# Optimization experiments

Measured on AMD Instinct MI355X. Metric: run time of the kernel, lower is better.

The kernel has to match this reference:

```python
import jax, jax.numpy as jnp
import numpy as np

D_MODEL = 768
NUM_HEADS = 12
HEAD_DIM = D_MODEL // NUM_HEADS


def _trunc_normal(key, shape, std):
    # truncated normal in [-3std, 3std], matching torch.nn.init.trunc_normal_
    return jax.random.truncated_normal(key, -3.0, 3.0, shape, dtype=jnp.float32) * std


def setup_inputs() -> dict:
    key = jax.random.key(0)
    kx, kq, kk, kv, ko = jax.random.split(key, 5)
    std = np.sqrt(2.0 / (D_MODEL + D_MODEL))
    x = jax.random.normal(kx, (4, 2048, D_MODEL), dtype=jnp.float32)
    Wq = _trunc_normal(kq, (D_MODEL, D_MODEL), std)
    Wk = _trunc_normal(kk, (D_MODEL, D_MODEL), std)
    Wv = _trunc_normal(kv, (D_MODEL, D_MODEL), std)
    Wo = _trunc_normal(ko, (D_MODEL, D_MODEL), std)
    return {"x": x, "Wq": Wq, "Wk": Wk, "Wv": Wv, "Wo": Wo}


def reference(x, Wq, Wk, Wv, Wo):
    b, s, _ = x.shape
    h, d = NUM_HEADS, HEAD_DIM
    # Linear: einsum 'b s i, o i -> b s o'
    Q = jnp.einsum('bsi,oi->bso', x, Wq).reshape(b, s, h, d).transpose(0, 2, 1, 3)
    K = jnp.einsum('bsi,oi->bso', x, Wk).reshape(b, s, h, d).transpose(0, 2, 1, 3)
    V = jnp.einsum('bsi,oi->bso', x, Wv).reshape(b, s, h, d).transpose(0, 2, 1, 3)
    scores = jnp.einsum('bhqd,bhkd->bhqk', Q, K) / jnp.sqrt(jnp.float32(d))
    causal = jnp.tril(jnp.ones((s, s), dtype=bool))  # (s, s)
    scores = jnp.where(causal, scores, jnp.float32(-jnp.inf))
    attn = jax.nn.softmax(scores, axis=-1)
    out = jnp.einsum('bhqk,bhkd->bhqd', attn, V)  # (b, h, s, d)
    out = out.transpose(0, 2, 1, 3).reshape(b, s, h * d)
    return jnp.einsum('bsi,oi->bso', out, Wo)
```

## Files before the change

### kernel.cpp

```cpp
#include <hip/hip_runtime.h>
#include <hip/hip_bf16.h>

#define SEQ   2048
#define BATCH 4
#define DM    768
#define NH    12
#define HD    64
#define MTOT  (BATCH*SEQ)

typedef short bf16x8 __attribute__((ext_vector_type(8)));
typedef float f32x4  __attribute__((ext_vector_type(4)));

static __device__ __forceinline__ short f2bf(float f) {
  union { __hip_bfloat16 h; short s; } u;
  u.h = __float2bfloat16(f);
  return u.s;
}

static __device__ __forceinline__ void async_cp16(const short* g, short* l) {
  __builtin_amdgcn_global_load_lds(
      (const __attribute__((address_space(1))) void*)g,
      (__attribute__((address_space(3))) void*)l, 16, 0, 0);
}

__global__ void cvt_kernel(const float* __restrict__ in, short* __restrict__ out, int n4) {
  int i = blockIdx.x * blockDim.x + threadIdx.x;
  if (i >= n4) return;
  float4 v = reinterpret_cast<const float4*>(in)[i];
  short4 o;
  o.x = f2bf(v.x); o.y = f2bf(v.y); o.z = f2bf(v.z); o.w = f2bf(v.w);
  reinterpret_cast<short4*>(out)[i] = o;
}

static __device__ __forceinline__ void gemm_lds_core(
    const short* __restrict__ A, const short* __restrict__ W,
    short* As, short* Bs, int m0, int n0, f32x4 acc[4][4])
{
  const int t = threadIdx.x;
  const int lane = t & 63, w = t >> 6;
  const int quad = lane >> 4, lq = lane & 15;
  const int mw = (w & 1) * 64, nw = (w >> 1) * 64;
  const int r0 = t >> 2, c0 = (t & 3) * 8;
  const short* ga0 = A + (size_t)(m0 + r0) * DM + c0;
  const short* ga1 = A + (size_t)(m0 + 64 + r0) * DM + c0;
  const short* gb0 = W + (size_t)(n0 + r0) * DM + c0;
  const short* gb1 = W + (size_t)(n0 + 64 + r0) * DM + c0;
  short* la0 = As + t * 8;
  short* la1 = As + 2048 + t * 8;
  short* lb0 = Bs + t * 8;
  short* lb1 = Bs + 2048 + t * 8;

  for (int k0 = 0; k0 < DM; k0 += 32) {
    async_cp16(ga0 + k0, la0);
    async_cp16(ga1 + k0, la1);
    async_cp16(gb0 + k0, lb0);
    async_cp16(gb1 + k0, lb1);
    __syncthreads();
    bf16x8 af[4], bf[4];
#pragma unroll
    for (int i = 0; i < 4; ++i) {
      af[i] = *(const bf16x8*)(As + (mw + i * 16 + lq) * 32 + quad * 8);
      bf[i] = *(const bf16x8*)(Bs + (nw + i * 16 + lq) * 32 + quad * 8);
    }
#pragma unroll
    for (int mt = 0; mt < 4; ++mt)
#pragma unroll
      for (int nt = 0; nt < 4; ++nt)
        acc[mt][nt] = __builtin_amdgcn_mfma_f32_16x16x32_bf16(af[mt], bf[nt], acc[mt][nt], 0, 0, 0);
    __syncthreads();
  }
}

__global__ __launch_bounds__(256) void qkv_gemm(
    const short* __restrict__ xb, const short* __restrict__ Wall,
    short* __restrict__ Qb, short* __restrict__ Kb, short* __restrict__ VTb)
{
  __shared__ __align__(16) short As[4096], Bs[4096];
  const int m0 = blockIdx.y * 128, n0 = blockIdx.x * 128;
  f32x4 acc[4][4] = {};
  gemm_lds_core(xb, Wall, As, Bs, m0, n0, acc);

  const int t = threadIdx.x;
  const int lane = t & 63, w = t >> 6;
  const int quad = lane >> 4, lq = lane & 15;
  const int mwb = m0 + (w & 1) * 64, nwb = n0 + (w >> 1) * 64;
#pragma unroll
  for (int mt = 0; mt < 4; ++mt)
#pragma unroll
    for (int nt = 0; nt < 4; ++nt) {
      const int n = nwb + nt * 16 + lq;
      const int z = n / DM, nn = n % DM;
      const int h = nn >> 6, d = nn & 63;
      const int mbase = mwb + mt * 16 + quad * 4;
      const int b = mbase >> 11, s0 = mbase & 2047;
      if (z == 2) {
        short4 v;
        v.x = f2bf(acc[mt][nt][0]); v.y = f2bf(acc[mt][nt][1]);
        v.z = f2bf(acc[mt][nt][2]); v.w = f2bf(acc[mt][nt][3]);
        *(short4*)(VTb + ((size_t)(b * NH + h) * HD + d) * SEQ + s0) = v;
      } else {
        short* dst = (z == 0) ? Qb : Kb;
#pragma unroll
        for (int r = 0; r < 4; ++r)
          dst[((size_t)(b * NH + h) * SEQ + s0 + r) * HD + d] = f2bf(acc[mt][nt][r]);
      }
    }
}

__global__ __launch_bounds__(256) void attn_kernel(
    const short* __restrict__ Qb, const short* __restrict__ Kb,
    const short* __restrict__ VTb, short* __restrict__ AOb)
{
  const int bp = blockIdx.x;
  const int bh = bp % 48;
  const int p  = bp / 48;
  const int w  = threadIdx.x >> 6;
  const int lane = threadIdx.x & 63;
  const int quad = lane >> 4, lq = lane & 15;
  int tile;
  if (w == 0) tile = 2 * p;
  else if (w == 1) tile = 63 - 2 * p;
  else if (w == 2) tile = 2 * p + 1;
  else tile = 62 - 2 * p;
  const int wq = tile * 32;
  const int b = bh / NH, h = bh % NH;

  const short* Qh = Qb  + (size_t)bh * SEQ * HD;
  const short* Kh = Kb  + (size_t)bh * SEQ * HD;
  const short* Vh = VTb + (size_t)bh * HD * SEQ;

  bf16x8 qf[2][2];
#pragma unroll
  for (int qt = 0; qt < 2; ++qt)
#pragma unroll
    for (int hh = 0; hh < 2; ++hh)
      qf[qt][hh] = *(const bf16x8*)(Qh + (size_t)(wq + qt * 16 + lq) * HD + hh * 32 + quad * 8);

  f32x4 o[4][2] = {};
  float m_[2] = {-3e38f, -3e38f};
  float l_[2] = {0.0f, 0.0f};
  const float C = 0.18033688011112042f;

  const int kend = wq + 32;
  for (int kb = 0; kb < kend; kb += 64) {
    f32x4 st[2][2][2] = {};
#pragma unroll
    for (int wd = 0; wd < 2; ++wd)
#pragma unroll
      for (int t = 0; t < 2; ++t) {
        const int krow = kb + 32 * wd + 8 * (lq >> 2) + 4 * t + (lq & 3);
        const short* kp = Kh + (size_t)krow * HD + quad * 8;
        bf16x8 k0 = *(const bf16x8*)(kp);
        bf16x8 k1 = *(const bf16x8*)(kp + 32);
        st[wd][t][0] = __builtin_amdgcn_mfma_f32_16x16x32_bf16(k0, qf[0][0], st[wd][t][0], 0, 0, 0);
        st[wd][t][0] = __builtin_amdgcn_mfma_f32_16x16x32_bf16(k1, qf[0][1], st[wd][t][0], 0, 0, 0);
        st[wd][t][1] = __builtin_amdgcn_mfma_f32_16x16x32_bf16(k0, qf[1][0], st[wd][t][1], 0, 0, 0);
        st[wd][t][1] = __builtin_amdgcn_mfma_f32_16x16x32_bf16(k1, qf[1][1], st[wd][t][1], 0, 0, 0);
      }

    float mx[2] = {-3e38f, -3e38f};
#pragma unroll
    for (int wd = 0; wd < 2; ++wd)
#pragma unroll
      for (int t = 0; t < 2; ++t)
#pragma unroll
        for (int qt = 0; qt < 2; ++qt)
#pragma unroll
          for (int r = 0; r < 4; ++r) {
            const int key = kb + 32 * wd + 8 * quad + 4 * t + r;
            const int q   = wq + qt * 16 + lq;
            const float v = (key <= q) ? st[wd][t][qt][r] : -3e38f;
            st[wd][t][qt][r] = v;
            mx[qt] = fmaxf(mx[qt], v);
          }
#pragma unroll
    for (int qt = 0; qt < 2; ++qt) {
      mx[qt] = fmaxf(mx[qt], __shfl_xor(mx[qt], 16));
      mx[qt] = fmaxf(mx[qt], __shfl_xor(mx[qt], 32));
    }

    float alpha[2], rs[2] = {0.0f, 0.0f};
#pragma unroll
    for (int qt = 0; qt < 2; ++qt) {
      const float mn = fmaxf(m_[qt], mx[qt]);
      alpha[qt] = __builtin_amdgcn_exp2f((m_[qt] - mn) * C);
      m_[qt] = mn;
    }
#pragma unroll
    for (int wd = 0; wd < 2; ++wd)
#pragma unroll
      for (int t = 0; t < 2; ++t)
#pragma unroll
        for (int qt = 0; qt < 2; ++qt)
#pragma unroll
          for (int r = 0; r < 4; ++r) {
            const float pv = __builtin_amdgcn_exp2f((st[wd][t][qt][r] - m_[qt]) * C);
            st[wd][t][qt][r] = pv;
            rs[qt] += pv;
          }
#pragma unroll
    for (int qt = 0; qt < 2; ++qt) {
      rs[qt] += __shfl_xor(rs[qt], 16);
      rs[qt] += __shfl_xor(rs[qt], 32);
      l_[qt] = l_[qt] * alpha[qt] + rs[qt];
    }
#pragma unroll
    for (int mt = 0; mt < 4; ++mt)
#pragma unroll
      for (int qt = 0; qt < 2; ++qt)
#pragma unroll
        for (int r = 0; r < 4; ++r)
          o[mt][qt][r] *= alpha[qt];

    bf16x8 pf[2][2];
#pragma unroll
    for (int wd = 0; wd < 2; ++wd)
#pragma unroll
      for (int qt = 0; qt < 2; ++qt) {
        bf16x8 f;
#pragma unroll
        for (int r = 0; r < 4; ++r) {
          f[r]     = f2bf(st[wd][0][qt][r]);
          f[r + 4] = f2bf(st[wd][1][qt][r]);
        }
        pf[wd][qt] = f;
      }

#pragma unroll
    for (int wd = 0; wd < 2; ++wd)
#pragma unroll
      for (int mt = 0; mt < 4; ++mt) {
        bf16x8 vf = *(const bf16x8*)(Vh + (size_t)(mt * 16 + lq) * SEQ + kb + 32 * wd + quad * 8);
        o[mt][0] = __builtin_amdgcn_mfma_f32_16x16x32_bf16(vf, pf[wd][0], o[mt][0], 0, 0, 0);
        o[mt][1] = __builtin_amdgcn_mfma_f32_16x16x32_bf16(vf, pf[wd][1], o[mt][1], 0, 0, 0);
      }
  }

#pragma unroll
  for (int qt = 0; qt < 2; ++qt) {
    const float inv = 1.0f / l_[qt];
    const int q = wq + qt * 16 + lq;
#pragma unroll
    for (int mt = 0; mt < 4; ++mt) {
      short4 v;
      v.x = f2bf(o[mt][qt][0] * inv);
      v.y = f2bf(o[mt][qt][1] * inv);
      v.z = f2bf(o[mt][qt][2] * inv);
      v.w = f2bf(o[mt][qt][3] * inv);
      *(short4*)(AOb + ((size_t)(b * SEQ + q)) * DM + h * HD + mt * 16 + quad * 4) = v;
    }
  }
}

__global__ __launch_bounds__(256) void out_gemm(
    const short* __restrict__ AOb, const short* __restrict__ Wob, float* __restrict__ C)
{
  __shared__ __align__(16) short As[4096], Bs[4096];
  const int m0 = blockIdx.y * 128, n0 = blockIdx.x * 128;
  f32x4 acc[4][4] = {};
  gemm_lds_core(AOb, Wob, As, Bs, m0, n0, acc);

  const int t = threadIdx.x;
  const int lane = t & 63, w = t >> 6;
  const int quad = lane >> 4, lq = lane & 15;
  const int mwb = m0 + (w & 1) * 64, nwb = n0 + (w >> 1) * 64;
#pragma unroll
  for (int mt = 0; mt < 4; ++mt)
#pragma unroll
    for (int nt = 0; nt < 4; ++nt) {
      const int n = nwb + nt * 16 + lq;
      const int mbase = mwb + mt * 16 + quad * 4;
#pragma unroll
      for (int r = 0; r < 4; ++r)
        C[(size_t)(mbase + r) * DM + n] = acc[mt][nt][r];
    }
}

extern "C" void kernel_launch(void* const* d_in, const int* in_sizes, int n_in,
                              void* d_out, int out_size, void* d_ws, size_t ws_size,
                              hipStream_t stream) {
  const float* x  = (const float*)d_in[0];
  const float* Wq = (const float*)d_in[1];
  const float* Wk = (const float*)d_in[2];
  const float* Wv = (const float*)d_in[3];
  const float* Wo = (const float*)d_in[4];
  float* out = (float*)d_out;

  short* xb  = (short*)d_ws;
  short* Wqb = xb  + (size_t)MTOT * DM;
  short* Wkb = Wqb + DM * DM;
  short* Wvb = Wkb + DM * DM;
  short* Wob = Wvb + DM * DM;
  short* Qb  = Wob + DM * DM;
  short* Kb  = Qb  + (size_t)MTOT * DM;
  short* VTb = Kb  + (size_t)MTOT * DM;
  short* AOb = xb;

  cvt_kernel<<<(MTOT * DM / 4 + 255) / 256, 256, 0, stream>>>(x, xb, MTOT * DM / 4);
  cvt_kernel<<<(DM * DM / 4 + 255) / 256, 256, 0, stream>>>(Wq, Wqb, DM * DM / 4);
  cvt_kernel<<<(DM * DM / 4 + 255) / 256, 256, 0, stream>>>(Wk, Wkb, DM * DM / 4);
  cvt_kernel<<<(DM * DM / 4 + 255) / 256, 256, 0, stream>>>(Wv, Wvb, DM * DM / 4);
  cvt_kernel<<<(DM * DM / 4 + 255) / 256, 256, 0, stream>>>(Wo, Wob, DM * DM / 4);

  qkv_gemm<<<dim3(3 * DM / 128, MTOT / 128), 256, 0, stream>>>(xb, Wqb, Qb, Kb, VTb);
  attn_kernel<<<dim3(768), 256, 0, stream>>>(Qb, Kb, VTb, AOb);
  out_gemm<<<dim3(DM / 128, MTOT / 128), 256, 0, stream>>>(AOb, Wob, out);
}
```

Before: 258.7 us.

## Share K/V tiles via LDS across warps in attention and fuse conversion kernels

The attention kernel now stages each 32-key K and V tile into shared memory with async global-to-LDS copies. All four warps in a block read the tile from there instead of each loading it from global memory. Each warp handles two 16-row query tiles, one near the start and one near the end of the sequence, to balance causal work. The five fp32-to-bf16 conversion launches are merged into one kernel to cut launch overhead. The cost is a __syncthreads pair per 32-key step and smaller per-warp query tiles, which lowers MFMA reuse per K load.

```diff
diff --git a/kernel.cpp b/kernel.cpp
--- a/kernel.cpp
+++ b/kernel.cpp
@@ -23,13 +23,22 @@
       (__attribute__((address_space(3))) void*)l, 16, 0, 0);
 }
 
-__global__ void cvt_kernel(const float* __restrict__ in, short* __restrict__ out, int n4) {
+__global__ void cvt5_kernel(const float* __restrict__ x, const float* __restrict__ wq,
+                            const float* __restrict__ wk, const float* __restrict__ wv,
+                            const float* __restrict__ wo, short* __restrict__ dst) {
+  const int NX4 = MTOT * DM / 4, NW4 = DM * DM / 4, TOT4 = NX4 + 4 * NW4;
   int i = blockIdx.x * blockDim.x + threadIdx.x;
-  if (i >= n4) return;
-  float4 v = reinterpret_cast<const float4*>(in)[i];
+  if (i >= TOT4) return;
+  const float* src; int off;
+  if (i < NX4) { src = x; off = i; }
+  else {
+    int j = i - NX4; int sel = j / NW4; off = j - sel * NW4;
+    src = (sel == 0) ? wq : (sel == 1) ? wk : (sel == 2) ? wv : wo;
+  }
+  float4 v = reinterpret_cast<const float4*>(src)[off];
   short4 o;
   o.x = f2bf(v.x); o.y = f2bf(v.y); o.z = f2bf(v.z); o.w = f2bf(v.w);
-  reinterpret_cast<short4*>(out)[i] = o;
+  reinterpret_cast<short4*>(dst)[i] = o;
 }
 
 static __device__ __forceinline__ void gemm_lds_core(
@@ -111,142 +120,172 @@
     const short* __restrict__ Qb, const short* __restrict__ Kb,
     const short* __restrict__ VTb, short* __restrict__ AOb)
 {
+  __shared__ __align__(16) short Ks[32 * 64];
+  __shared__ __align__(16) short Vs[64 * 32];
   const int bp = blockIdx.x;
   const int bh = bp % 48;
-  const int p  = bp / 48;
-  const int w  = threadIdx.x >> 6;
-  const int lane = threadIdx.x & 63;
+  const int g  = bp / 48;
+  const int tid = threadIdx.x;
+  const int w = tid >> 6, lane = tid & 63;
   const int quad = lane >> 4, lq = lane & 15;
-  int tile;
-  if (w == 0) tile = 2 * p;
-  else if (w == 1) tile = 63 - 2 * p;
-  else if (w == 2) tile = 2 * p + 1;
-  else tile = 62 - 2 * p;
-  const int wq = tile * 32;
+  const int tp = 4 * g + w;
   const int b = bh / NH, h = bh % NH;
+  const int q0b = 16 * tp;
+  const int q1b = 2032 - 16 * tp;
+  const int E0 = q0b + 16;
+  const int E1 = q1b + 16;
+  const int Eblk = 2048 - 64 * g;
 
   const short* Qh = Qb  + (size_t)bh * SEQ * HD;
   const short* Kh = Kb  + (size_t)bh * SEQ * HD;
   const short* Vh = VTb + (size_t)bh * HD * SEQ;
 
-  bf16x8 qf[2][2];
-#pragma unroll
-  for (int qt = 0; qt < 2; ++qt)
-#pragma unroll
-    for (int hh = 0; hh < 2; ++hh)
-      qf[qt][hh] = *(const bf16x8*)(Qh + (size_t)(wq + qt * 16 + lq) * HD + hh * 32 + quad * 8);
-
-  f32x4 o[4][2] = {};
-  float m_[2] = {-3e38f, -3e38f};
-  float l_[2] = {0.0f, 0.0f};
-  const float C = 0.18033688011112042f;
-
-  const int kend = wq + 32;
-  for (int kb = 0; kb < kend; kb += 64) {
-    f32x4 st[2][2][2] = {};
-#pragma unroll
-    for (int wd = 0; wd < 2; ++wd)
-#pragma unroll
-      for (int t = 0; t < 2; ++t) {
-        const int krow = kb + 32 * wd + 8 * (lq >> 2) + 4 * t + (lq & 3);
-        const short* kp = Kh + (size_t)krow * HD + quad * 8;
-        bf16x8 k0 = *(const bf16x8*)(kp);
-        bf16x8 k1 = *(const bf16x8*)(kp + 32);
-        st[wd][t][0] = __builtin_amdgcn_mfma_f32_16x16x32_bf16(k0, qf[0][0], st[wd][t][0], 0, 0, 0);
-        st[wd][t][0] = __builtin_amdgcn_mfma_f32_16x16x32_bf16(k1, qf[0][1], st[wd][t][0], 0, 0, 0);
-        st[wd][t][1] = __builtin_amdgcn_mfma_f32_16x16x32_bf16(k0, qf[1][0], st[wd][t][1], 0, 0, 0);
-        st[wd][t][1] = __builtin_amdgcn_mfma_f32_16x16x32_bf16(k1, qf[1][1], st[wd][t][1], 0, 0, 0);
-      }
-
-    float mx[2] = {-3e38f, -3e38f};
-#pragma unroll
-    for (int wd = 0; wd < 2; ++wd)
-#pragma unroll
-      for (int t = 0; t < 2; ++t)
-#pragma unroll
-        for (int qt = 0; qt < 2; ++qt)
+  bf16x8 qf0[2], qf1[2];
+#pragma unroll
+  for (int hh = 0; hh < 2; ++hh) {
+    qf0[hh] = *(const bf16x8*)(Qh + (size_t)(q0b + lq) * HD + hh * 32 + quad * 8);
+    qf1[hh] = *(const bf16x8*)(Qh + (size_t)(q1b + lq) * HD + hh * 32 + quad * 8);
+  }
+
+  f32x4 o0[4] = {}, o1[4] = {};
+  float m0v = -3e38f, m1v = -3e38f;
+  float l0v = 0.0f, l1v = 0.0f;
+  const float Cc = 0.18033688011112042f;
+
+  const short* gK = Kh + (size_t)(tid >> 3) * HD + (tid & 7) * 8;
+  const short* gV = Vh + (size_t)(tid >> 2) * SEQ + (tid & 3) * 8;
+  short* lK = Ks + tid * 8;
+  short* lV = Vs + tid * 8;
+
+  for (int kb = 0; kb < Eblk; kb += 32) {
+    async_cp16(gK + (size_t)kb * HD, lK);
+    async_cp16(gV + kb, lV);
+    __syncthreads();
+    if (kb < E1) {
+      const bool act0 = kb < E0;
+      f32x4 st0[2] = {}, st1[2] = {};
+#pragma unroll
+      for (int t2 = 0; t2 < 2; ++t2) {
+        const int row = 8 * (lq >> 2) + 4 * t2 + (lq & 3);
+        bf16x8 k0 = *(const bf16x8*)(Ks + row * 64 + quad * 8);
+        bf16x8 k1 = *(const bf16x8*)(Ks + row * 64 + 32 + quad * 8);
+        st1[t2] = __builtin_amdgcn_mfma_f32_16x16x32_bf16(k0, qf1[0], st1[t2], 0, 0, 0);
+        st1[t2] = __builtin_amdgcn_mfma_f32_16x16x32_bf16(k1, qf1[1], st1[t2], 0, 0, 0);
+        if (act0) {
+          st0[t2] = __builtin_amdgcn_mfma_f32_16x16x32_bf16(k0, qf0[0], st0[t2], 0, 0, 0);
+          st0[t2] = __builtin_amdgcn_mfma_f32_16x16x32_bf16(k1, qf0[1], st0[t2], 0, 0, 0);
+        }
+      }
+      bf16x8 vf[4];
+#pragma unroll
+      for (int mt = 0; mt < 4; ++mt)
+        vf[mt] = *(const bf16x8*)(Vs + (mt * 16 + lq) * 32 + quad * 8);
+
+      bf16x8 pf1;
+      {
+        const int qv = q1b + lq;
+        float mx = -3e38f;
+#pragma unroll
+        for (int t2 = 0; t2 < 2; ++t2)
 #pragma unroll
           for (int r = 0; r < 4; ++r) {
-            const int key = kb + 32 * wd + 8 * quad + 4 * t + r;
-            const int q   = wq + qt * 16 + lq;
-            const float v = (key <= q) ? st[wd][t][qt][r] : -3e38f;
-            st[wd][t][qt][r] = v;
-            mx[qt] = fmaxf(mx[qt], v);
+            const int key = kb + 8 * quad + 4 * t2 + r;
+            const float v = (key <= qv) ? st1[t2][r] : -3e38f;
+            st1[t2][r] = v;
+            mx = fmaxf(mx, v);
           }
-#pragma unroll
-    for (int qt = 0; qt < 2; ++qt) {
-      mx[qt] = fmaxf(mx[qt], __shfl_xor(mx[qt], 16));
-      mx[qt] = fmaxf(mx[qt], __shfl_xor(mx[qt], 32));
-    }
-
-    float alpha[2], rs[2] = {0.0f, 0.0f};
-#pragma unroll
-    for (int qt = 0; qt < 2; ++qt) {
-      const float mn = fmaxf(m_[qt], mx[qt]);
-      alpha[qt] = __builtin_amdgcn_exp2f((m_[qt] - mn) * C);
-      m_[qt] = mn;
-    }
-#pragma unroll
-    for (int wd = 0; wd < 2; ++wd)
-#pragma unroll
-      for (int t = 0; t < 2; ++t)
-#pragma unroll
-        for (int qt = 0; qt < 2; ++qt)
+        mx = fmaxf(mx, __shfl_xor(mx, 16));
+        mx = fmaxf(mx, __shfl_xor(mx, 32));
+        const float mn = fmaxf(m1v, mx);
+        const float al = __builtin_amdgcn_exp2f((m1v - mn) * Cc);
+        m1v = mn;
+        float rs = 0.0f;
+#pragma unroll
+        for (int t2 = 0; t2 < 2; ++t2)
 #pragma unroll
           for (int r = 0; r < 4; ++r) {
-            const float pv = __builtin_amdgcn_exp2f((st[wd][t][qt][r] - m_[qt]) * C);
-            st[wd][t][qt][r] = pv;
-            rs[qt] += pv;
+            const float p = __builtin_amdgcn_exp2f((st1[t2][r] - mn) * Cc);
+            rs += p;
+            pf1[t2 * 4 + r] = f2bf(p);
           }
-#pragma unroll
-    for (int qt = 0; qt < 2; ++qt) {
-      rs[qt] += __shfl_xor(rs[qt], 16);
-      rs[qt] += __shfl_xor(rs[qt], 32);
-      l_[qt] = l_[qt] * alpha[qt] + rs[qt];
-    }
-#pragma unroll
-    for (int mt = 0; mt < 4; ++mt)
-#pragma unroll
-      for (int qt = 0; qt < 2; ++qt)
-#pragma unroll
-        for (int r = 0; r < 4; ++r)
-          o[mt][qt][r] *= alpha[qt];
-
-    bf16x8 pf[2][2];
-#pragma unroll
-    for (int wd = 0; wd < 2; ++wd)
-#pragma unroll
-      for (int qt = 0; qt < 2; ++qt) {
-        bf16x8 f;
-#pragma unroll
-        for (int r = 0; r < 4; ++r) {
-          f[r]     = f2bf(st[wd][0][qt][r]);
-          f[r + 4] = f2bf(st[wd][1][qt][r]);
-        }
-        pf[wd][qt] = f;
-      }
-
-#pragma unroll
-    for (int wd = 0; wd < 2; ++wd)
+        rs += __shfl_xor(rs, 16);
+        rs += __shfl_xor(rs, 32);
+        l1v = l1v * al + rs;
+#pragma unroll
+        for (int mt = 0; mt < 4; ++mt)
+#pragma unroll
+          for (int r = 0; r < 4; ++r)
+            o1[mt][r] *= al;
+      }
+      bf16x8 pf0;
+      if (act0) {
+        const int qv = q0b + lq;
+        float mx = -3e38f;
+#pragma unroll
+        for (int t2 = 0; t2 < 2; ++t2)
+#pragma unroll
+          for (int r = 0; r < 4; ++r) {
+            const int key = kb + 8 * quad + 4 * t2 + r;
+            const float v = (key <= qv) ? st0[t2][r] : -3e38f;
+            st0[t2][r] = v;
+            mx = fmaxf(mx, v);
+          }
+        mx = fmaxf(mx, __shfl_xor(mx, 16));
+        mx = fmaxf(mx, __shfl_xor(mx, 32));
+        const float mn = fmaxf(m0v, mx);
+        const float al = __builtin_amdgcn_exp2f((m0v - mn) * Cc);
+        m0v = mn;
+        float rs = 0.0f;
+#pragma unroll
+        for (int t2 = 0; t2 < 2; ++t2)
+#pragma unroll
+          for (int r = 0; r < 4; ++r) {
+            const float p = __builtin_amdgcn_exp2f((st0[t2][r] - mn) * Cc);
+            rs += p;
+            pf0[t2 * 4 + r] = f2bf(p);
+          }
+        rs += __shfl_xor(rs, 16);
+        rs += __shfl_xor(rs, 32);
+        l0v = l0v * al + rs;
+#pragma unroll
+        for (int mt = 0; mt < 4; ++mt)
+#pragma unroll
+          for (int r = 0; r < 4; ++r)
+            o0[mt][r] *= al;
+      }
 #pragma unroll
       for (int mt = 0; mt < 4; ++mt) {
-        bf16x8 vf = *(const bf16x8*)(Vh + (size_t)(mt * 16 + lq) * SEQ + kb + 32 * wd + quad * 8);
-        o[mt][0] = __builtin_amdgcn_mfma_f32_16x16x32_bf16(vf, pf[wd][0], o[mt][0], 0, 0, 0);
-        o[mt][1] = __builtin_amdgcn_mfma_f32_16x16x32_bf16(vf, pf[wd][1], o[mt][1], 0, 0, 0);
-      }
-  }
-
-#pragma unroll
-  for (int qt = 0; qt < 2; ++qt) {
-    const float inv = 1.0f / l_[qt];
-    const int q = wq + qt * 16 + lq;
+        o1[mt] = __builtin_amdgcn_mfma_f32_16x16x32_bf16(vf[mt], pf1, o1[mt], 0, 0, 0);
+        if (act0)
+          o0[mt] = __builtin_amdgcn_mfma_f32_16x16x32_bf16(vf[mt], pf0, o0[mt], 0, 0, 0);
+      }
+    }
+    __syncthreads();
+  }
+
+  {
+    const float inv = 1.0f / l1v;
+    const int q = q1b + lq;
 #pragma unroll
     for (int mt = 0; mt < 4; ++mt) {
       short4 v;
-      v.x = f2bf(o[mt][qt][0] * inv);
-      v.y = f2bf(o[mt][qt][1] * inv);
-      v.z = f2bf(o[mt][qt][2] * inv);
-      v.w = f2bf(o[mt][qt][3] * inv);
+      v.x = f2bf(o1[mt][0] * inv);
+      v.y = f2bf(o1[mt][1] * inv);
+      v.z = f2bf(o1[mt][2] * inv);
+      v.w = f2bf(o1[mt][3] * inv);
+      *(short4*)(AOb + ((size_t)(b * SEQ + q)) * DM + h * HD + mt * 16 + quad * 4) = v;
+    }
+  }
+  {
+    const float inv = 1.0f / l0v;
+    const int q = q0b + lq;
+#pragma unroll
+    for (int mt = 0; mt < 4; ++mt) {
+      short4 v;
+      v.x = f2bf(o0[mt][0] * inv);
+      v.y = f2bf(o0[mt][1] * inv);
+      v.z = f2bf(o0[mt][2] * inv);
+      v.w = f2bf(o0[mt][3] * inv);
       *(short4*)(AOb + ((size_t)(b * SEQ + q)) * DM + h * HD + mt * 16 + quad * 4) = v;
     }
   }
@@ -296,11 +335,8 @@
   short* VTb = Kb  + (size_t)MTOT * DM;
   short* AOb = xb;
 
-  cvt_kernel<<<(MTOT * DM / 4 + 255) / 256, 256, 0, stream>>>(x, xb, MTOT * DM / 4);
-  cvt_kernel<<<(DM * DM / 4 + 255) / 256, 256, 0, stream>>>(Wq, Wqb, DM * DM / 4);
-  cvt_kernel<<<(DM * DM / 4 + 255) / 256, 256, 0, stream>>>(Wk, Wkb, DM * DM / 4);
-  cvt_kernel<<<(DM * DM / 4 + 255) / 256, 256, 0, stream>>>(Wv, Wvb, DM * DM / 4);
-  cvt_kernel<<<(DM * DM / 4 + 255) / 256, 256, 0, stream>>>(Wo, Wob, DM * DM / 4);
+  const int TOT4 = (MTOT * DM + 4 * DM * DM) / 4;
+  cvt5_kernel<<<(TOT4 + 255) / 256, 256, 0, stream>>>(x, Wq, Wk, Wv, Wo, xb);
 
   qkv_gemm<<<dim3(3 * DM / 128, MTOT / 128), 256, 0, stream>>>(xb, Wqb, Qb, Kb, VTb);
   attn_kernel<<<dim3(768), 256, 0, stream>>>(Qb, Kb, VTb, AOb);
```

Measured after the change: 241.0 us. 1.07x faster.
